# Kernel optimization log

Measured on AMD Instinct MI355X. Metric: run time of the kernel, lower is better.

Reference implementation:

```python
import jax, jax.numpy as jnp
import numpy as np

B, SEQ, H = 256, 200, 256
NFFT, HOP = 16, 8
FREQ = NFFT // 2 + 1          # 9
NSEG = SEQ // HOP + 1         # 26 (SEQ % HOP == 0 -> pad_len == 0)
FACTOR = 2


def _gelu(x):
    return jax.nn.gelu(x, approximate=False)  # torch nn.GELU / F.gelu default = exact erf


def _layernorm(x, w, b, eps=1e-12):
    u = x.mean(-1, keepdims=True)
    s = ((x - u) ** 2).mean(-1, keepdims=True)
    return w * (x - u) / jnp.sqrt(s + eps) + b


def _mixer(xr, xi, w1, b1, w2, b2):
    # complex MLP: einsum '...ijk,jkl->...ijl' with per-kept-dim weights
    e = lambda a, w: jnp.einsum('bijk,jkl->bijl', a, w)
    o1r = _gelu(e(xr, w1[0]) - e(xi, w1[1]) + b1[0])
    o1i = _gelu(e(xi, w1[0]) + e(xr, w1[1]) + b1[1])
    o2r = e(o1r, w2[0]) - e(o1i, w2[1]) + b2[0]
    # NOTE: faithful to the source bug: o1_image used in BOTH terms of o2_image
    o2i = e(o1i, w2[0]) + e(o1i, w2[1]) + b2[1]
    return o2r, o2i


def _stft(x):
    # torch.stft(n_fft=NFFT, hop=HOP, center=True, onesided=True, normalized=True,
    #            pad_mode='constant', window=None -> rectangular ones)
    pad = NFFT // 2
    xp = jnp.pad(x, ((0, 0), (pad, pad)))
    idx = jnp.arange(NSEG)[:, None] * HOP + jnp.arange(NFFT)[None, :]
    frames = xp[:, idx]                                    # [N, NSEG, NFFT]
    spec = jnp.fft.rfft(frames, axis=-1) * (NFFT ** -0.5)  # normalized=True
    return jnp.swapaxes(spec, -1, -2)                      # [N, FREQ, NSEG]


def _istft(spec):
    # torch.istft(center=True, normalized=True, rectangular window)
    n = spec.shape[0]
    frames = jnp.fft.irfft(jnp.swapaxes(spec, -1, -2) * (NFFT ** 0.5), n=NFFT, axis=-1)
    L = (NSEG - 1) * HOP + NFFT
    idx = (jnp.arange(NSEG)[:, None] * HOP + jnp.arange(NFFT)[None, :]).ravel()
    y = jnp.zeros((n, L), frames.dtype).at[:, idx].add(frames.reshape(n, -1))
    env = jnp.zeros((L,), frames.dtype).at[idx].add(1.0)   # window**2 overlap-add
    pad = NFFT // 2
    out_len = (NSEG - 1) * HOP                              # = SEQ
    return y[:, pad:pad + out_len] / env[pad:pad + out_len]


def setup_inputs() -> dict:
    key = jax.random.key(0)
    ks = jax.random.split(key, 24)
    p = lambda k, sh: jax.random.normal(k, sh, jnp.float32) * 0.02
    d = {}
    d["input_tensor"] = jax.random.normal(ks[0], (B, SEQ, H), jnp.float32)
    # grouped conv2d: weight [NSEG, 1, H, FREQ] -> stored as [NSEG, H, FREQ]
    d["conv_w"] = p(ks[1], (NSEG, H, FREQ)); d["conv_b"] = p(ks[2], (NSEG,))
    d["fm_w1"] = p(ks[3], (2, NSEG, FREQ, FREQ * FACTOR)); d["fm_b1"] = p(ks[4], (2, NSEG, FREQ * FACTOR))
    d["fm_w2"] = p(ks[5], (2, NSEG, FREQ * FACTOR, FREQ)); d["fm_b2"] = p(ks[6], (2, NSEG, FREQ))
    d["cm_w1"] = p(ks[7], (2, NSEG, H, H * FACTOR)); d["cm_b1"] = p(ks[8], (2, NSEG, H * FACTOR))
    d["cm_w2"] = p(ks[9], (2, NSEG, H * FACTOR, H)); d["cm_b2"] = p(ks[10], (2, NSEG, H))
    d["sm_w1"] = p(ks[11], (2, FREQ, NSEG, NSEG * FACTOR)); d["sm_b1"] = p(ks[12], (2, FREQ, NSEG * FACTOR))
    d["sm_w2"] = p(ks[13], (2, FREQ, NSEG * FACTOR, NSEG)); d["sm_b2"] = p(ks[14], (2, FREQ, NSEG))
    d["ln_w"] = jnp.ones((H,), jnp.float32); d["ln_b"] = jnp.zeros((H,), jnp.float32)
    d["ff_w1"] = p(ks[15], (H, 4 * H)); d["ff_b1"] = p(ks[16], (4 * H,))
    d["ff_w2"] = p(ks[17], (4 * H, H)); d["ff_b2"] = p(ks[18], (H,))
    d["ff_ln_w"] = jnp.ones((H,), jnp.float32); d["ff_ln_b"] = jnp.zeros((H,), jnp.float32)
    return d


def reference(input_tensor, conv_w, conv_b, fm_w1, fm_b1, fm_w2, fm_b2,
              cm_w1, cm_b1, cm_w2, cm_b2, sm_w1, sm_b1, sm_w2, sm_b2,
              ln_w, ln_b, ff_w1, ff_b1, ff_w2, ff_b2, ff_ln_w, ff_ln_b):
    b, seq, h = input_tensor.shape
    x = jnp.swapaxes(input_tensor, -1, -2).reshape(b * h, seq)  # pad_len == 0
    spec = _stft(x).reshape(b, h, FREQ, NSEG)
    xr, xi = spec.real, spec.imag
    xnorm = jnp.sqrt(xr ** 2 + xi ** 2)                         # [b,h,F,S]
    # grouped conv2d with full (H,FREQ) kernel == per-segment weighted sum
    w = jnp.einsum('bhfs,shf->bs', xnorm, conv_w) + conv_b
    w = w + jnp.exp(jnp.arange(1 - NSEG, 1, dtype=jnp.float32))  # exp decay bias
    xr = xr * w[:, None, None, :]
    xi = xi * w[:, None, None, :]
    # -> [b,h,S,F]: frequency mixing (kept=segment, mixed=freq)
    xr = jnp.swapaxes(xr, -1, -2); xi = jnp.swapaxes(xi, -1, -2)
    xr, xi = _mixer(xr, xi, fm_w1, fm_b1, fm_w2, fm_b2)
    # -> [b,F,S,h]: channel mixing (kept=segment, mixed=hidden)
    xr = jnp.swapaxes(xr, 1, 3); xi = jnp.swapaxes(xi, 1, 3)
    xr, xi = _mixer(xr, xi, cm_w1, cm_b1, cm_w2, cm_b2)
    # -> [b,h,F,S]: segment mixing (kept=freq, mixed=segment)
    xr = jnp.transpose(xr, (0, 3, 1, 2)); xi = jnp.transpose(xi, (0, 3, 1, 2))
    xr, xi = _mixer(xr, xi, sm_w1, sm_b1, sm_w2, sm_b2)
    spec = (xr + 1j * xi).reshape(b * h, FREQ, NSEG)
    y = _istft(spec)[:, :seq].reshape(b, h, seq)
    y = jnp.swapaxes(y, -1, -2)                                  # [b,seq,h]
    hs = _layernorm(y + input_tensor, ln_w, ln_b)                # dropout p=0
    ff = _gelu(hs @ ff_w1 + ff_b1) @ ff_w2 + ff_b2
    return _layernorm(ff + hs, ff_ln_w, ff_ln_b)
```

## Files before the change

kernel.cpp:

```cpp
#include <hip/hip_runtime.h>
#include <hip/hip_bf16.h>
#include <math.h>

typedef __hip_bfloat16 bf16;
typedef short bf16x8 __attribute__((ext_vector_type(8)));
typedef float f32x4 __attribute__((ext_vector_type(4)));

#define B_    256
#define SEQ_  200
#define H_    256
#define FREQ_ 9
#define NSEG_ 26
#define LDS64 64

__device__ __forceinline__ float ldb(const bf16* p, size_t i){ return __bfloat162float(p[i]); }
__device__ __forceinline__ void stb(bf16* p, size_t i, float v){ p[i] = __float2bfloat16(v); }
__device__ __forceinline__ short f2b(float v){ union{bf16 b; short s;} c; c.b = __float2bfloat16(v); return c.s; }
__device__ __forceinline__ float gelu_(float x){ return 0.5f*x*(1.0f+erff(x*0.7071067811865475f)); }

__device__ __constant__ float CT16[16] = {
  1.0f, 0.9238795325f, 0.7071067812f, 0.3826834324f, 0.0f, -0.3826834324f, -0.7071067812f, -0.9238795325f,
 -1.0f,-0.9238795325f,-0.7071067812f,-0.3826834324f, 0.0f,  0.3826834324f, 0.7071067812f,  0.9238795325f};
__device__ __constant__ float ST16[16] = {
  0.0f, 0.3826834324f, 0.7071067812f, 0.9238795325f, 1.0f,  0.9238795325f, 0.7071067812f,  0.3826834324f,
  0.0f,-0.3826834324f,-0.7071067812f,-0.9238795325f,-1.0f, -0.9238795325f,-0.7071067812f, -0.3826834324f};

__device__ __forceinline__ void gload16(const short* g, short* l){
  __builtin_amdgcn_global_load_lds(
      (const __attribute__((address_space(1))) unsigned int*)(const void*)g,
      (__attribute__((address_space(3))) unsigned int*)(void*)l, 16, 0, 0);
}

template<int ROWS>
__device__ __forceinline__ void stage_tile(short* lds, const short* src, int rstride, int tid){
  int rl = tid >> 3;
  int c  = tid & 7;
  #pragma unroll
  for(int p=0; p<ROWS/32; p++){
    int r = p*32 + rl;
    int csrc = c ^ (r & 7);
    gload16(src + (size_t)r*rstride + csrc*8, lds + r*LDS64 + c*8);
  }
}

__device__ __forceinline__ void mma_bk64(const short* lA, const short* lB, int wm, int wn,
                                         int lane, f32x4 acc[4][4]){
  int m_l = lane & 15, quad = lane >> 4;
  int sw = m_l & 7;
  #pragma unroll
  for(int ks=0; ks<64; ks+=32){
    int cs = (((ks>>3) + quad) ^ sw) * 8;
    bf16x8 a[4], b[4];
    #pragma unroll
    for(int i=0;i<4;i++) a[i] = *(const bf16x8*)&lA[(wm + i*16 + m_l)*LDS64 + cs];
    #pragma unroll
    for(int j=0;j<4;j++) b[j] = *(const bf16x8*)&lB[(wn + j*16 + m_l)*LDS64 + cs];
    #pragma unroll
    for(int i=0;i<4;i++)
      #pragma unroll
      for(int j=0;j<4;j++)
        acc[i][j] = __builtin_amdgcn_mfma_f32_16x16x32_bf16(a[i], b[j], acc[i][j], 0,0,0);
  }
}

__global__ __launch_bounds__(256) void k_prep_b1(const float* __restrict__ w1, short* __restrict__ B1t){
  int g = blockIdx.x;
  int jt = g & 7, ht = (g>>3)&3, p = (g>>5)&1, s = g>>6;
  __shared__ float tile[64][65];
  int t = threadIdx.x;
  const float* src = w1 + (size_t)p*3407872 + (size_t)s*131072;
  #pragma unroll
  for(int q=0;q<16;q++){
    int r = q*4 + (t>>6), c = t & 63;
    tile[r][c] = src[(size_t)(ht*64 + r)*512 + jt*64 + c];
  }
  __syncthreads();
  int n_l = t >> 2, kc = (t & 3)*16;
  short tA[16] __attribute__((aligned(16)));
  short tB[16] __attribute__((aligned(16)));
  #pragma unroll
  for(int i=0;i<16;i++){
    float v = tile[kc+i][n_l];
    tA[i] = (p==0) ? f2b(v) : f2b(-v);
    tB[i] = f2b(v);
  }
  int j = jt*64 + n_l, h = ht*64 + kc;
  size_t d1, d2;
  if(p==0){ d1 = ((size_t)(s*1024 + j))*512 + h;
            d2 = ((size_t)(s*1024 + 512 + j))*512 + 256 + h; }
  else    { d1 = ((size_t)(s*1024 + j))*512 + 256 + h;
            d2 = ((size_t)(s*1024 + 512 + j))*512 + h; }
  *(int4*)&B1t[d1] = *(int4*)&tA[0]; *(int4*)&B1t[d1+8] = *(int4*)&tA[8];
  *(int4*)&B1t[d2] = *(int4*)&tB[0]; *(int4*)&B1t[d2+8] = *(int4*)&tB[8];
}

__global__ __launch_bounds__(256) void k_prep_b2(const float* __restrict__ w2,
                                                 short* __restrict__ B2r, short* __restrict__ B2i){
  int g = blockIdx.x;
  int ht = g & 3, jt = (g>>2)&7, s = g>>5;
  __shared__ float t0[64][65], t1[64][65];
  int t = threadIdx.x;
  const float* s0 = w2 + (size_t)s*131072;
  const float* s1 = w2 + 3407872 + (size_t)s*131072;
  #pragma unroll
  for(int q=0;q<16;q++){
    int r = q*4 + (t>>6), c = t & 63;
    t0[r][c] = s0[(size_t)(jt*64 + r)*256 + ht*64 + c];
    t1[r][c] = s1[(size_t)(jt*64 + r)*256 + ht*64 + c];
  }
  __syncthreads();
  int n_l = t >> 2, jc = (t & 3)*16;
  short ta[16] __attribute__((aligned(16)));
  short tb[16] __attribute__((aligned(16)));
  short tc[16] __attribute__((aligned(16)));
  #pragma unroll
  for(int i=0;i<16;i++){
    float v0 = t0[jc+i][n_l], v1 = t1[jc+i][n_l];
    ta[i] = f2b(v0); tb[i] = f2b(-v1); tc[i] = f2b(v0+v1);
  }
  int n = ht*64 + n_l, j = jt*64 + jc;
  size_t dr = ((size_t)(s*256 + n))*1024 + j;
  size_t di = ((size_t)(s*256 + n))*512 + j;
  *(int4*)&B2r[dr]     = *(int4*)&ta[0]; *(int4*)&B2r[dr+8]     = *(int4*)&ta[8];
  *(int4*)&B2r[dr+512] = *(int4*)&tb[0]; *(int4*)&B2r[dr+520]   = *(int4*)&tb[8];
  *(int4*)&B2i[di]     = *(int4*)&tc[0]; *(int4*)&B2i[di+8]     = *(int4*)&tc[8];
}

__global__ __launch_bounds__(256) void k_transp(const float* __restrict__ src, short* __restrict__ dst,
                                                int R, int C){
  int ct = blockIdx.x % (C/64);
  int rt = blockIdx.x / (C/64);
  __shared__ float tile[64][65];
  int t = threadIdx.x;
  #pragma unroll
  for(int p=0;p<16;p++){
    int r = p*4 + (t>>6), c = t & 63;
    tile[r][c] = src[(size_t)(rt*64 + r)*C + ct*64 + c];
  }
  __syncthreads();
  int row_out = t >> 2, rc = (t & 3)*16;
  short tmp[16] __attribute__((aligned(16)));
  #pragma unroll
  for(int i=0;i<16;i++) tmp[i] = f2b(tile[rc+i][row_out]);
  size_t base = (size_t)(ct*64 + row_out)*R + rt*64 + rc;
  *(int4*)&dst[base] = *(int4*)&tmp[0]; *(int4*)&dst[base+8] = *(int4*)&tmp[8];
}

__global__ __launch_bounds__(256) void k_prep_sm(const float* __restrict__ w1, const float* __restrict__ w2,
                                                 short* __restrict__ B1sm, short* __restrict__ B2sm){
  int f = blockIdx.x;
  int t = threadIdx.x;
  for(int idx=t; idx<8192; idx+=256){
    int jp = idx >> 6, k = idx & 63;
    float v = 0.f;
    if(jp < 104){
      int j = (jp < 52) ? jp : jp - 52;
      if(k < 26){
        int s = k;
        v = (jp < 52) ? w1[f*1352 + s*52 + j] : w1[12168 + f*1352 + s*52 + j];
      } else if(k >= 32 && k < 58){
        int s = k - 32;
        v = (jp < 52) ? -w1[12168 + f*1352 + s*52 + j] : w1[f*1352 + s*52 + j];
      }
    }
    B1sm[(size_t)f*8192 + idx] = f2b(v);
  }
  for(int idx=t; idx<8192; idx+=256){
    int sop = idx >> 7, k = idx & 127;
    float v = 0.f;
    if(sop < 26){
      if(k < 52)       v = w2[f*1352 + k*26 + sop];
      else if(k < 104) v = -w2[12168 + f*1352 + (k-52)*26 + sop];
    } else if(sop < 52){
      int so = sop - 26;
      if(k >= 52 && k < 104)
        v = w2[f*1352 + (k-52)*26 + so] + w2[12168 + f*1352 + (k-52)*26 + so];
    }
    B2sm[(size_t)f*8192 + idx] = f2b(v);
  }
}

__global__ __launch_bounds__(256) void k_sfm(const float* __restrict__ inp,
                                             const float* __restrict__ cw, const float* __restrict__ cb,
                                             const float* __restrict__ w1, const float* __restrict__ bb1,
                                             const float* __restrict__ w2, const float* __restrict__ bb2,
                                             bf16* __restrict__ oR, bf16* __restrict__ oI){
  int blk = blockIdx.x; int b = blk / NSEG_; int s = blk % NSEG_; int h = threadIdx.x;
  __shared__ float2 lw1[162], lw2[162], lb1[18], lb2[9];
  __shared__ float red[256];
  for(int i=h; i<162; i+=256){
    lw1[i] = make_float2(w1[s*162+i], w1[4212 + s*162+i]);
    lw2[i] = make_float2(w2[s*162+i], w2[4212 + s*162+i]);
  }
  if(h < 18) lb1[h] = make_float2(bb1[s*18+h], bb1[468 + s*18+h]);
  if(h < 9)  lb2[h] = make_float2(bb2[s*9+h],  bb2[234 + s*9+h]);

  float xv[16];
  int t0 = s*8 - 8;
  #pragma unroll
  for(int k=0;k<16;k++){
    int t = t0 + k;
    xv[k] = (t>=0 && t<SEQ_) ? inp[(size_t)(b*SEQ_+t)*H_ + h] : 0.0f;
  }
  float xr[9], xi[9];
  float acc = 0.f;
  #pragma unroll
  for(int f=0;f<FREQ_;f++){
    float ar=0.f, ai=0.f;
    #pragma unroll
    for(int k=0;k<16;k++){
      int m = (f*k) & 15;
      ar += xv[k]*CT16[m];
      ai -= xv[k]*ST16[m];
    }
    xr[f] = 0.25f*ar; xi[f] = 0.25f*ai;
    acc += sqrtf(xr[f]*xr[f] + xi[f]*xi[f]) * cw[(s*H_+h)*FREQ_ + f];
  }

  red[h] = acc; __syncthreads();
  for(int off=128; off>0; off>>=1){ if(h<off) red[h] += red[h+off]; __syncthreads(); }
  float wv = red[0] + cb[s] + __expf((float)(s - (NSEG_-1)));
  #pragma unroll
  for(int f=0;f<9;f++){ xr[f] *= wv; xi[f] *= wv; }

  float gr[18], gi[18];
  #pragma unroll
  for(int j=0;j<18;j++){
    float hr = lb1[j].x, hi = lb1[j].y;
    #pragma unroll
    for(int f=0;f<9;f++){
      float2 ww = lw1[f*18+j];
      hr += xr[f]*ww.x - xi[f]*ww.y;
      hi += xi[f]*ww.x + xr[f]*ww.y;
    }
    gr[j] = gelu_(hr); gi[j] = gelu_(hi);
  }
  #pragma unroll
  for(int f=0;f<9;f++){
    float orr = lb2[f].x, oii = lb2[f].y;
    #pragma unroll
    for(int j=0;j<18;j++){
      float2 ww = lw2[j*9+f];
      orr += gr[j]*ww.x - gi[j]*ww.y;
      oii += gi[j]*ww.x + gi[j]*ww.y;
    }
    size_t o = ((size_t)(s*B_+b)*FREQ_+f)*H_ + h;
    stb(oR, o, orr); stb(oI, o, oii);
  }
}

__global__ __launch_bounds__(256) void k_cm1(const bf16* __restrict__ Xr, const bf16* __restrict__ Xi,
                                             const short* __restrict__ B1t, const float* __restrict__ b1bias,
                                             short* __restrict__ H, int half){
  int nt = blockIdx.x & 7, mt = (blockIdx.x >> 3) % 9, s = blockIdx.x / 72;
  int tid = threadIdx.x, lane = tid & 63, wave = tid >> 6;
  int wm = (wave & 1)*64, wn = (wave >> 1)*64;
  __shared__ __align__(16) short lA[128*LDS64];
  __shared__ __align__(16) short lB[128*LDS64];
  f32x4 acc[4][4];
  #pragma unroll
  for(int i=0;i<4;i++)
    #pragma unroll
    for(int j=0;j<4;j++) acc[i][j] = (f32x4){0.f,0.f,0.f,0.f};
  int rowbase = half*1152 + mt*128;
  const short* Bbase = B1t + ((size_t)(s*1024 + nt*128))*512;
  for(int k0=0; k0<512; k0+=64){
    const short* Asrc = (k0 < 256)
      ? (const short*)(Xr + ((size_t)(s*2304 + rowbase))*256 + k0)
      : (const short*)(Xi + ((size_t)(s*2304 + rowbase))*256 + (k0-256));
    stage_tile<128>(lA, Asrc, 256, tid);
    stage_tile<128>(lB, Bbase + k0, 512, tid);
    __syncthreads();
    mma_bk64(lA, lB, wm, wn, lane, acc);
    __syncthreads();
  }
  int m_l = lane & 15, quad = lane >> 4;
  #pragma unroll
  for(int i=0;i<4;i++){
    #pragma unroll
    for(int j=0;j<4;j++){
      int n = nt*128 + wn + j*16 + m_l;
      float bias = (n < 512) ? b1bias[s*512 + n] : b1bias[13312 + s*512 + (n-512)];
      #pragma unroll
      for(int r=0;r<4;r++){
        int mrow = wm + i*16 + quad*4 + r;
        float v = gelu_(acc[i][j][r] + bias);
        H[((size_t)(s*1152 + mt*128 + mrow))*1024 + n] = f2b(v);
      }
    }
  }
}

__global__ __launch_bounds__(256) void k_cm2(const short* __restrict__ H,
                                             const short* __restrict__ B2r, const short* __restrict__ B2i,
                                             const float* __restrict__ b2bias,
                                             bf16* __restrict__ oR, bf16* __restrict__ oI, int half){
  int nt = blockIdx.x & 3, mt = (blockIdx.x>>2) % 9, s = blockIdx.x / 36;
  int tid = threadIdx.x, lane = tid & 63, wave = tid >> 6;
  int wm = (wave & 1)*64, wn = (wave >> 1)*64;
  bool isOi = nt >= 2;
  int n0 = (nt & 1)*128;
  int K = isOi ? 512 : 1024;
  int Aoff = isOi ? 512 : 0;
  int Bstride = isOi ? 512 : 1024;
  const short* Bb = isOi ? (B2i + ((size_t)(s*256 + n0))*512) : (B2r + ((size_t)(s*256 + n0))*1024);
  const short* Ab = H + ((size_t)(s*1152 + mt*128))*1024 + Aoff;
  __shared__ __align__(16) short lA[128*LDS64];
  __shared__ __align__(16) short lB[128*LDS64];
  f32x4 acc[4][4];
  #pragma unroll
  for(int i=0;i<4;i++)
    #pragma unroll
    for(int j=0;j<4;j++) acc[i][j] = (f32x4){0.f,0.f,0.f,0.f};
  for(int k0=0; k0<K; k0+=64){
    stage_tile<128>(lA, Ab + k0, 1024, tid);
    stage_tile<128>(lB, Bb + k0, Bstride, tid);
    __syncthreads();
    mma_bk64(lA, lB, wm, wn, lane, acc);
    __syncthreads();
  }
  int m_l = lane & 15, quad = lane >> 4;
  bf16* outp = isOi ? oI : oR;
  #pragma unroll
  for(int i=0;i<4;i++){
    #pragma unroll
    for(int j=0;j<4;j++){
      int n = n0 + wn + j*16 + m_l;
      float bias = b2bias[(isOi ? 6656 : 0) + s*256 + n];
      #pragma unroll
      for(int r=0;r<4;r++){
        int mrow = wm + i*16 + quad*4 + r;
        int rowg = half*1152 + mt*128 + mrow;
        stb(outp, ((size_t)rowg*NSEG_ + s)*256 + n, acc[i][j][r] + bias);
      }
    }
  }
}

#define LDX 72
#define LDG 136
__global__ __launch_bounds__(256) void k_smm(const bf16* __restrict__ iR, const bf16* __restrict__ iI,
                                             const short* __restrict__ B1sm, const short* __restrict__ B2sm,
                                             const float* __restrict__ bb1, const float* __restrict__ bb2,
                                             bf16* __restrict__ oR, bf16* __restrict__ oI){
  int blk = blockIdx.x;
  int f  = blk % 9;
  int hh = (blk/9) & 1;
  int bq = blk / 18;
  int t = threadIdx.x, lane = t & 63, wave = t >> 6;
  int m_l = lane & 15, quad = lane >> 4;
  __shared__ __align__(16) short sm[18432 + 8704];
  __shared__ float lb1[128];
  short* lX  = sm;
  short* lB1 = sm + 128*LDX;
  short* lG  = sm;
  short* lB2 = sm + 18432;
  int rbase = (bq*9 + f)*26;

  #pragma unroll
  for(int it=0; it<4; it++){
    int idx = it*256 + t;
    int r = idx >> 3, c = idx & 7;
    *(int4*)&lB1[r*LDX + c*8] = *(const int4*)&B1sm[(size_t)f*8192 + r*64 + c*8];
  }
  #pragma unroll
  for(int it=0; it<4; it++){
    int idx = it*256 + t;
    int r = idx >> 4, c = idx & 15;
    *(int4*)&lB2[r*LDG + c*8] = *(const int4*)&B2sm[(size_t)f*8192 + r*128 + c*8];
  }
  if(t < 128) lb1[t] = (t < 52) ? bb1[f*52 + t] : (t < 104 ? bb1[468 + f*52 + (t-52)] : 0.f);

  int hl = t & 127, g = t >> 7;
  #pragma unroll
  for(int it=0; it<13; it++){
    int a   = it*2 + g;
    int arr = a >= 13;
    int pr  = arr ? a-13 : a;
    int s0  = pr*2;
    const bf16* src = arr ? iI : iR;
    unsigned v0 = *(const unsigned short*)&src[((size_t)(rbase+s0  ))*256 + hh*128 + hl];
    unsigned v1 = *(const unsigned short*)&src[((size_t)(rbase+s0+1))*256 + hh*128 + hl];
    *(unsigned*)&lX[hl*LDX + arr*32 + s0] = v0 | (v1 << 16);
  }
  {
    int zb = g ? 58 : 26;
    #pragma unroll
    for(int i=0;i<3;i++) *(unsigned*)&lX[hl*LDX + zb + i*2] = 0u;
  }
  __syncthreads();

  int h0 = wave*32;
  f32x4 acc1[2][8];
  #pragma unroll
  for(int i=0;i<2;i++)
    #pragma unroll
    for(int j=0;j<8;j++) acc1[i][j] = (f32x4){0.f,0.f,0.f,0.f};
  #pragma unroll
  for(int ks=0; ks<64; ks+=32){
    bf16x8 av[2], bv[8];
    #pragma unroll
    for(int i=0;i<2;i++) av[i] = *(const bf16x8*)&lX[(h0 + i*16 + m_l)*LDX + ks + quad*8];
    #pragma unroll
    for(int j=0;j<8;j++) bv[j] = *(const bf16x8*)&lB1[(j*16 + m_l)*LDX + ks + quad*8];
    #pragma unroll
    for(int i=0;i<2;i++)
      #pragma unroll
      for(int j=0;j<8;j++)
        acc1[i][j] = __builtin_amdgcn_mfma_f32_16x16x32_bf16(av[i], bv[j], acc1[i][j], 0,0,0);
  }
  __syncthreads();

  #pragma unroll
  for(int i=0;i<2;i++){
    #pragma unroll
    for(int j=0;j<8;j++){
      int jp = j*16 + m_l;
      float bias = lb1[jp];
      #pragma unroll
      for(int r=0;r<4;r++){
        int hrow = h0 + i*16 + quad*4 + r;
        lG[hrow*LDG + jp] = f2b(gelu_(acc1[i][j][r] + bias));
      }
    }
  }
  __syncthreads();

  f32x4 acc2[2][4];
  #pragma unroll
  for(int i=0;i<2;i++)
    #pragma unroll
    for(int j=0;j<4;j++) acc2[i][j] = (f32x4){0.f,0.f,0.f,0.f};
  #pragma unroll
  for(int ks=0; ks<128; ks+=32){
    bf16x8 av[2], bv[4];
    #pragma unroll
    for(int i=0;i<2;i++) av[i] = *(const bf16x8*)&lG[(h0 + i*16 + m_l)*LDG + ks + quad*8];
    #pragma unroll
    for(int j=0;j<4;j++) bv[j] = *(const bf16x8*)&lB2[(j*16 + m_l)*LDG + ks + quad*8];
    #pragma unroll
    for(int i=0;i<2;i++)
      #pragma unroll
      for(int j=0;j<4;j++)
        acc2[i][j] = __builtin_amdgcn_mfma_f32_16x16x32_bf16(av[i], bv[j], acc2[i][j], 0,0,0);
  }

  #pragma unroll
  for(int j=0;j<4;j++){
    int sop = j*16 + m_l;
    if(sop < 52){
      int arr = sop >= 26;
      int so  = sop - (arr ? 26 : 0);
      float bias = bb2[(arr ? 234 : 0) + f*26 + so];
      bf16* outp = arr ? oI : oR;
      #pragma unroll
      for(int i=0;i<2;i++){
        int h = hh*128 + h0 + i*16 + quad*4;
        short pk[4] __attribute__((aligned(8)));
        #pragma unroll
        for(int r=0;r<4;r++) pk[r] = f2b(acc2[i][j][r] + bias);
        *(int2*)&outp[((size_t)(rbase + so))*256 + h] = *(const int2*)&pk[0];
      }
    }
  }
}

__global__ __launch_bounds__(256) void k_ist(const bf16* __restrict__ iR, const bf16* __restrict__ iI,
                                             const float* __restrict__ inp,
                                             const float* __restrict__ lnw, const float* __restrict__ lnb,
                                             float* __restrict__ hs, bf16* __restrict__ hsb){
  int blk = blockIdx.x; int b = blk / SEQ_; int t = blk % SEQ_; int h = threadIdx.x;
  int l = t + 8;
  int s2 = l >> 3, k2 = l & 7;
  int s1 = s2 - 1, k1 = k2 + 8;
  float acc = 0.f;
  #pragma unroll
  for(int p=0;p<2;p++){
    int s = p ? s2 : s1;
    int k = p ? k2 : k1;
    size_t base = (size_t)(b*FREQ_)*NSEG_;
    float v = ldb(iR, (base + 0*NSEG_ + s)*256 + h);
    float a8 = ldb(iR, (base + 8*NSEG_ + s)*256 + h);
    v += (k & 1) ? -a8 : a8;
    #pragma unroll
    for(int f=1;f<8;f++){
      int m = (f*k) & 15;
      float rr = ldb(iR, (base + f*NSEG_ + s)*256 + h);
      float ii = ldb(iI, (base + f*NSEG_ + s)*256 + h);
      v += 2.f*(rr*CT16[m] - ii*ST16[m]);
    }
    acc += 0.25f*v;
  }
  float z = 0.5f*acc + inp[(size_t)(b*SEQ_+t)*H_ + h];

  __shared__ float red[256];
  red[h] = z; __syncthreads();
  for(int off=128; off>0; off>>=1){ if(h<off) red[h] += red[h+off]; __syncthreads(); }
  float u = red[0] * (1.f/256.f);
  __syncthreads();
  float d = z - u;
  red[h] = d*d; __syncthreads();
  for(int off=128; off>0; off>>=1){ if(h<off) red[h] += red[h+off]; __syncthreads(); }
  float var = red[0] * (1.f/256.f);
  float o = lnw[h]*d*rsqrtf(var + 1e-12f) + lnb[h];
  size_t oi = (size_t)(b*SEQ_+t)*H_ + h;
  hs[oi] = o;
  stb(hsb, oi, o);
}

__global__ __launch_bounds__(256) void k_ff1m(const short* __restrict__ hsb, const short* __restrict__ fw1t,
                                              const float* __restrict__ fb1, short* __restrict__ hid, int row0){
  int nt = blockIdx.x & 7, mt = blockIdx.x >> 3;
  int tid = threadIdx.x, lane = tid & 63, wave = tid >> 6;
  int wm = (wave & 1)*64, wn = (wave >> 1)*64;
  __shared__ __align__(16) short lA[128*LDS64];
  __shared__ __align__(16) short lB[128*LDS64];
  f32x4 acc[4][4];
  #pragma unroll
  for(int i=0;i<4;i++)
    #pragma unroll
    for(int j=0;j<4;j++) acc[i][j] = (f32x4){0.f,0.f,0.f,0.f};
  const short* Ab = hsb + ((size_t)(row0 + mt*128))*256;
  const short* Bb = fw1t + ((size_t)(nt*128))*256;
  for(int k0=0; k0<256; k0+=64){
    stage_tile<128>(lA, Ab + k0, 256, tid);
    stage_tile<128>(lB, Bb + k0, 256, tid);
    __syncthreads();
    mma_bk64(lA, lB, wm, wn, lane, acc);
    __syncthreads();
  }
  int m_l = lane & 15, quad = lane >> 4;
  #pragma unroll
  for(int i=0;i<4;i++){
    #pragma unroll
    for(int j=0;j<4;j++){
      int n = nt*128 + wn + j*16 + m_l;
      float bias = fb1[n];
      #pragma unroll
      for(int r=0;r<4;r++){
        int mrow = wm + i*16 + quad*4 + r;
        hid[((size_t)(mt*128 + mrow))*1024 + n] = f2b(gelu_(acc[i][j][r] + bias));
      }
    }
  }
}

__global__ __launch_bounds__(256) void k_ff2m(const short* __restrict__ hid, const short* __restrict__ fw2t,
                                              const float* __restrict__ fb2, const float* __restrict__ hs,
                                              const float* __restrict__ lnw, const float* __restrict__ lnb,
                                              float* __restrict__ out, int row0){
  int mt = blockIdx.x;
  int tid = threadIdx.x, lane = tid & 63, wave = tid >> 6;
  int wn = wave*64;
  __shared__ __align__(16) short lA[64*LDS64];
  __shared__ __align__(16) short lB[256*LDS64];
  __shared__ float ssum[64][4], ssq[64][4];
  f32x4 acc[4][4];
  #pragma unroll
  for(int i=0;i<4;i++)
    #pragma unroll
    for(int j=0;j<4;j++) acc[i][j] = (f32x4){0.f,0.f,0.f,0.f};
  const short* Ab = hid + ((size_t)(mt*64))*1024;
  for(int k0=0; k0<1024; k0+=64){
    stage_tile<64>(lA, Ab + k0, 1024, tid);
    stage_tile<256>(lB, fw2t + k0, 1024, tid);
    __syncthreads();
    mma_bk64(lA, lB, 0, wn, lane, acc);
    __syncthreads();
  }
  int m_l = lane & 15, quad = lane >> 4;
  int rowg0 = row0 + mt*64;
  #pragma unroll
  for(int i=0;i<4;i++){
    #pragma unroll
    for(int j=0;j<4;j++){
      int col = wn + j*16 + m_l;
      float bias = fb2[col];
      #pragma unroll
      for(int r=0;r<4;r++){
        int mrow = i*16 + quad*4 + r;
        acc[i][j][r] += bias + hs[(size_t)(rowg0+mrow)*256 + col];
      }
    }
  }
  #pragma unroll
  for(int i=0;i<4;i++){
    #pragma unroll
    for(int r=0;r<4;r++){
      float sv = 0.f, sq = 0.f;
      #pragma unroll
      for(int j=0;j<4;j++){ float v = acc[i][j][r]; sv += v; sq += v*v; }
      #pragma unroll
      for(int msk=1; msk<16; msk<<=1){ sv += __shfl_xor(sv, msk); sq += __shfl_xor(sq, msk); }
      if(m_l == 0){ int mrow = i*16 + quad*4 + r; ssum[mrow][wave] = sv; ssq[mrow][wave] = sq; }
    }
  }
  __syncthreads();
  if(tid < 64){
    float s1 = ssum[tid][0]+ssum[tid][1]+ssum[tid][2]+ssum[tid][3];
    float s2 = ssq[tid][0]+ssq[tid][1]+ssq[tid][2]+ssq[tid][3];
    float mean = s1*(1.f/256.f);
    float var  = s2*(1.f/256.f) - mean*mean;
    ssum[tid][0] = mean;
    ssq[tid][0]  = rsqrtf(var + 1e-12f);
  }
  __syncthreads();
  #pragma unroll
  for(int i=0;i<4;i++){
    #pragma unroll
    for(int j=0;j<4;j++){
      int col = wn + j*16 + m_l;
      float gw = lnw[col], gb = lnb[col];
      #pragma unroll
      for(int r=0;r<4;r++){
        int mrow = i*16 + quad*4 + r;
        float mean = ssum[mrow][0], inv = ssq[mrow][0];
        out[(size_t)(rowg0+mrow)*256 + col] = (acc[i][j][r] - mean)*inv*gw + gb;
      }
    }
  }
}

extern "C" void kernel_launch(void* const* d_in, const int* in_sizes, int n_in,
                              void* d_out, int out_size, void* d_ws, size_t ws_size,
                              hipStream_t stream){
  const float* inp    = (const float*)d_in[0];
  const float* conv_w = (const float*)d_in[1];
  const float* conv_b = (const float*)d_in[2];
  const float* fm_w1  = (const float*)d_in[3];
  const float* fm_b1  = (const float*)d_in[4];
  const float* fm_w2  = (const float*)d_in[5];
  const float* fm_b2  = (const float*)d_in[6];
  const float* cm_w1  = (const float*)d_in[7];
  const float* cm_b1  = (const float*)d_in[8];
  const float* cm_w2  = (const float*)d_in[9];
  const float* cm_b2  = (const float*)d_in[10];
  const float* sm_w1  = (const float*)d_in[11];
  const float* sm_b1  = (const float*)d_in[12];
  const float* sm_w2  = (const float*)d_in[13];
  const float* sm_b2  = (const float*)d_in[14];
  const float* ln_w   = (const float*)d_in[15];
  const float* ln_b   = (const float*)d_in[16];
  const float* ff_w1  = (const float*)d_in[17];
  const float* ff_b1  = (const float*)d_in[18];
  const float* ff_w2  = (const float*)d_in[19];
  const float* ff_b2  = (const float*)d_in[20];
  const float* ffln_w = (const float*)d_in[21];
  const float* ffln_b = (const float*)d_in[22];
  float* out = (float*)d_out;

  const size_t NS = (size_t)B_ * NSEG_ * FREQ_ * H_;
  const size_t HN = (size_t)NSEG_ * 1152 * 1024;
  short* ws = (short*)d_ws;
  bf16*  b0   = (bf16*)ws;
  bf16*  b1   = (bf16*)(ws + NS);
  bf16*  b2   = (bf16*)(ws + 2*NS);
  bf16*  b3   = (bf16*)(ws + 3*NS);
  short* H    = ws + 4*NS;
  short* B1t  = H + HN;
  short* B2r  = B1t + (size_t)26*1024*512;
  short* B2i  = B2r + (size_t)26*256*1024;
  short* fw1t = B2i + (size_t)26*256*512;
  short* fw2t = fw1t + 262144;
  short* B1sm = fw2t + 262144;
  short* B2sm = B1sm + 73728;
  float* hs   = (float*)b0;
  bf16*  hsb  = (bf16*)H;
  short* hid  = (short*)b2;

  k_prep_b1<<<1664, 256, 0, stream>>>(cm_w1, B1t);
  k_prep_b2<<<832,  256, 0, stream>>>(cm_w2, B2r, B2i);
  k_transp <<<64,   256, 0, stream>>>(ff_w1, fw1t, 256, 1024);
  k_transp <<<64,   256, 0, stream>>>(ff_w2, fw2t, 1024, 256);
  k_prep_sm<<<9,    256, 0, stream>>>(sm_w1, sm_w2, B1sm, B2sm);

  k_sfm<<<B_*NSEG_, 256, 0, stream>>>(inp, conv_w, conv_b, fm_w1, fm_b1, fm_w2, fm_b2, b2, b3);
  for(int half=0; half<2; half++){
    k_cm1<<<26*72, 256, 0, stream>>>(b2, b3, B1t, cm_b1, H, half);
    k_cm2<<<26*36, 256, 0, stream>>>(H, B2r, B2i, cm_b2, b0, b1, half);
  }
  k_smm<<<B_*2*FREQ_, 256, 0, stream>>>(b0, b1, B1sm, B2sm, sm_b1, sm_b2, b2, b3);
  k_ist<<<B_*SEQ_,  256, 0, stream>>>(b2, b3, inp, ln_w, ln_b, hs, hsb);
  for(int c=0; c<2; c++){
    int row0 = c*25600;
    k_ff1m<<<1600, 256, 0, stream>>>((const short*)hsb, fw1t, ff_b1, hid, row0);
    k_ff2m<<<400,  256, 0, stream>>>(hid, fw2t, ff_b2, hs, ffln_w, ffln_b, out, row0);
  }
}
```

Measured before the change: 953.1 us.

## Move frequency-mixer complex MLP onto bf16 MFMA with prepacked real-block weights

Replaces the scalar per-thread complex MLP in the STFT/frequency-mix kernel with two small bf16 MFMA GEMMs. Activations are staged through LDS, and the complex weights come from a new prep kernel that packs them into real block matrices, including the source bug's o2i term. The aim is to cut the large FP32 FMA count per thread. In exchange it adds LDS traffic, extra barriers, bf16 rounding of the intermediates, and zero-padded K/N dimensions (18→32, 36→64).

```diff
diff --git a/kernel.cpp b/kernel.cpp
--- a/kernel.cpp
+++ b/kernel.cpp
@@ -16,6 +16,7 @@
 __device__ __forceinline__ float ldb(const bf16* p, size_t i){ return __bfloat162float(p[i]); }
 __device__ __forceinline__ void stb(bf16* p, size_t i, float v){ p[i] = __float2bfloat16(v); }
 __device__ __forceinline__ short f2b(float v){ union{bf16 b; short s;} c; c.b = __float2bfloat16(v); return c.s; }
+__device__ __forceinline__ unsigned short f2bu(float v){ union{bf16 b; unsigned short s;} c; c.b = __float2bfloat16(v); return c.s; }
 __device__ __forceinline__ float gelu_(float x){ return 0.5f*x*(1.0f+erff(x*0.7071067811865475f)); }
 
 __device__ __constant__ float CT16[16] = {
@@ -180,27 +181,75 @@
   }
 }
 
-__global__ __launch_bounds__(256) void k_sfm(const float* __restrict__ inp,
-                                             const float* __restrict__ cw, const float* __restrict__ cb,
-                                             const float* __restrict__ w1, const float* __restrict__ bb1,
-                                             const float* __restrict__ w2, const float* __restrict__ bb2,
-                                             bf16* __restrict__ oR, bf16* __restrict__ oI){
-  int blk = blockIdx.x; int b = blk / NSEG_; int s = blk % NSEG_; int h = threadIdx.x;
-  __shared__ float2 lw1[162], lw2[162], lb1[18], lb2[9];
+__global__ __launch_bounds__(256) void k_prep_fm(const float* __restrict__ w1, const float* __restrict__ w2,
+                                                 short* __restrict__ B1fm, short* __restrict__ B2fm){
+  int s = blockIdx.x;
+  int t = threadIdx.x;
+  for(int idx=t; idx<1536; idx+=256){
+    int n = idx >> 5, k = idx & 31;
+    float v = 0.f;
+    if(n < 18){
+      if(k < 9)       v = w1[s*162 + k*18 + n];
+      else if(k < 18) v = -w1[4212 + s*162 + (k-9)*18 + n];
+    } else if(n < 36){
+      int j = n - 18;
+      if(k < 9)       v = w1[4212 + s*162 + k*18 + j];
+      else if(k < 18) v = w1[s*162 + (k-9)*18 + j];
+    }
+    B1fm[s*1536 + idx] = f2b(v);
+  }
+  for(int idx=t; idx<2048; idx+=256){
+    int n = idx >> 6, k = idx & 63;
+    float v = 0.f;
+    if(n < 9){
+      if(k < 18)      v = w2[s*162 + k*9 + n];
+      else if(k < 36) v = -w2[4212 + s*162 + (k-18)*9 + n];
+    } else if(n < 18){
+      int f = n - 9;
+      if(k >= 18 && k < 36)
+        v = w2[s*162 + (k-18)*9 + f] + w2[4212 + s*162 + (k-18)*9 + f];
+    }
+    B2fm[s*2048 + idx] = f2b(v);
+  }
+}
+
+#define LX1 40
+#define LG1 72
+__global__ __launch_bounds__(256) void k_sfm2(const float* __restrict__ inp,
+                                              const float* __restrict__ cw, const float* __restrict__ cb,
+                                              const short* __restrict__ B1fm, const short* __restrict__ B2fm,
+                                              const float* __restrict__ bb1, const float* __restrict__ bb2,
+                                              bf16* __restrict__ oR, bf16* __restrict__ oI){
+  int blk = blockIdx.x; int b = blk / NSEG_; int s = blk % NSEG_; int t = threadIdx.x;
+  int lane = t & 63, wave = t >> 6, m_l = lane & 15, quad = lane >> 4;
+  __shared__ __align__(16) short sm[20736];
   __shared__ float red[256];
-  for(int i=h; i<162; i+=256){
-    lw1[i] = make_float2(w1[s*162+i], w1[4212 + s*162+i]);
-    lw2[i] = make_float2(w2[s*162+i], w2[4212 + s*162+i]);
-  }
-  if(h < 18) lb1[h] = make_float2(bb1[s*18+h], bb1[468 + s*18+h]);
-  if(h < 9)  lb2[h] = make_float2(bb2[s*9+h],  bb2[234 + s*9+h]);
+  __shared__ float lb1f[48];
+  short* lX  = sm;
+  short* lB1 = sm + 10240;
+  short* lG  = sm;
+  short* lB2 = sm + 18432;
+
+  {
+    const short* src1 = B1fm + s*1536;
+    for(int idx=t; idx<768; idx+=256){
+      int r = idx >> 4, c = idx & 15;
+      *(unsigned*)&lB1[r*LX1 + c*2] = *(const unsigned*)&src1[r*32 + c*2];
+    }
+    const short* src2 = B2fm + s*2048;
+    for(int idx=t; idx<1024; idx+=256){
+      int r = idx >> 5, c = idx & 31;
+      *(unsigned*)&lB2[r*LG1 + c*2] = *(const unsigned*)&src2[r*64 + c*2];
+    }
+    if(t < 48) lb1f[t] = (t < 18) ? bb1[s*18 + t] : (t < 36 ? bb1[468 + s*18 + (t-18)] : 0.f);
+  }
 
   float xv[16];
   int t0 = s*8 - 8;
   #pragma unroll
   for(int k=0;k<16;k++){
-    int t = t0 + k;
-    xv[k] = (t>=0 && t<SEQ_) ? inp[(size_t)(b*SEQ_+t)*H_ + h] : 0.0f;
+    int tt = t0 + k;
+    xv[k] = (tt>=0 && tt<SEQ_) ? inp[(size_t)(b*SEQ_+tt)*H_ + t] : 0.0f;
   }
   float xr[9], xi[9];
   float acc = 0.f;
@@ -214,38 +263,101 @@
       ai -= xv[k]*ST16[m];
     }
     xr[f] = 0.25f*ar; xi[f] = 0.25f*ai;
-    acc += sqrtf(xr[f]*xr[f] + xi[f]*xi[f]) * cw[(s*H_+h)*FREQ_ + f];
-  }
-
-  red[h] = acc; __syncthreads();
-  for(int off=128; off>0; off>>=1){ if(h<off) red[h] += red[h+off]; __syncthreads(); }
+    acc += sqrtf(xr[f]*xr[f] + xi[f]*xi[f]) * cw[(s*H_+t)*FREQ_ + f];
+  }
+
+  red[t] = acc; __syncthreads();
+  for(int off=128; off>0; off>>=1){ if(t<off) red[t] += red[t+off]; __syncthreads(); }
   float wv = red[0] + cb[s] + __expf((float)(s - (NSEG_-1)));
-  #pragma unroll
-  for(int f=0;f<9;f++){ xr[f] *= wv; xi[f] *= wv; }
-
-  float gr[18], gi[18];
-  #pragma unroll
-  for(int j=0;j<18;j++){
-    float hr = lb1[j].x, hi = lb1[j].y;
-    #pragma unroll
-    for(int f=0;f<9;f++){
-      float2 ww = lw1[f*18+j];
-      hr += xr[f]*ww.x - xi[f]*ww.y;
-      hi += xi[f]*ww.x + xr[f]*ww.y;
-    }
-    gr[j] = gelu_(hr); gi[j] = gelu_(hi);
-  }
-  #pragma unroll
-  for(int f=0;f<9;f++){
-    float orr = lb2[f].x, oii = lb2[f].y;
-    #pragma unroll
-    for(int j=0;j<18;j++){
-      float2 ww = lw2[j*9+f];
-      orr += gr[j]*ww.x - gi[j]*ww.y;
-      oii += gi[j]*ww.x + gi[j]*ww.y;
-    }
-    size_t o = ((size_t)(s*B_+b)*FREQ_+f)*H_ + h;
-    stb(oR, o, orr); stb(oI, o, oii);
+
+  {
+    float vb[32];
+    #pragma unroll
+    for(int f=0;f<9;f++){ vb[f] = xr[f]*wv; vb[9+f] = xi[f]*wv; }
+    #pragma unroll
+    for(int k=18;k<32;k++) vb[k] = 0.f;
+    #pragma unroll
+    for(int c=0;c<16;c++){
+      unsigned u = (unsigned)f2bu(vb[2*c]) | ((unsigned)f2bu(vb[2*c+1]) << 16);
+      *(unsigned*)&lX[t*LX1 + c*2] = u;
+    }
+  }
+  __syncthreads();
+
+  int h0 = wave*64;
+  f32x4 acc1[4][3];
+  #pragma unroll
+  for(int i=0;i<4;i++)
+    #pragma unroll
+    for(int j=0;j<3;j++) acc1[i][j] = (f32x4){0.f,0.f,0.f,0.f};
+  {
+    bf16x8 a1[4], b1v[3];
+    #pragma unroll
+    for(int i=0;i<4;i++) a1[i] = *(const bf16x8*)&lX[(h0 + i*16 + m_l)*LX1 + quad*8];
+    #pragma unroll
+    for(int j=0;j<3;j++) b1v[j] = *(const bf16x8*)&lB1[(j*16 + m_l)*LX1 + quad*8];
+    #pragma unroll
+    for(int i=0;i<4;i++)
+      #pragma unroll
+      for(int j=0;j<3;j++)
+        acc1[i][j] = __builtin_amdgcn_mfma_f32_16x16x32_bf16(a1[i], b1v[j], acc1[i][j], 0,0,0);
+  }
+  __syncthreads();
+
+  #pragma unroll
+  for(int i=0;i<4;i++){
+    #pragma unroll
+    for(int j=0;j<3;j++){
+      int n = j*16 + m_l;
+      float bias = lb1f[n];
+      #pragma unroll
+      for(int r=0;r<4;r++){
+        int row = h0 + i*16 + quad*4 + r;
+        lG[row*LG1 + n] = f2b(gelu_(acc1[i][j][r] + bias));
+      }
+    }
+  }
+  #pragma unroll
+  for(int c=0;c<8;c++) *(unsigned*)&lG[t*LG1 + 48 + c*2] = 0u;
+  __syncthreads();
+
+  f32x4 acc2[4][2];
+  #pragma unroll
+  for(int i=0;i<4;i++)
+    #pragma unroll
+    for(int j=0;j<2;j++) acc2[i][j] = (f32x4){0.f,0.f,0.f,0.f};
+  #pragma unroll
+  for(int ks=0; ks<64; ks+=32){
+    bf16x8 a2[4], b2v[2];
+    #pragma unroll
+    for(int i=0;i<4;i++) a2[i] = *(const bf16x8*)&lG[(h0 + i*16 + m_l)*LG1 + ks + quad*8];
+    #pragma unroll
+    for(int j=0;j<2;j++) b2v[j] = *(const bf16x8*)&lB2[(j*16 + m_l)*LG1 + ks + quad*8];
+    #pragma unroll
+    for(int i=0;i<4;i++)
+      #pragma unroll
+      for(int j=0;j<2;j++)
+        acc2[i][j] = __builtin_amdgcn_mfma_f32_16x16x32_bf16(a2[i], b2v[j], acc2[i][j], 0,0,0);
+  }
+
+  #pragma unroll
+  for(int j=0;j<2;j++){
+    int n = j*16 + m_l;
+    if(n < 18){
+      bool isI = n >= 9;
+      int f = isI ? n-9 : n;
+      float bias = isI ? bb2[234 + s*9 + f] : bb2[s*9 + f];
+      bf16* outp = isI ? oI : oR;
+      size_t base = ((size_t)(s*B_ + b)*FREQ_ + f)*H_;
+      #pragma unroll
+      for(int i=0;i<4;i++){
+        int h = h0 + i*16 + quad*4;
+        short pk[4] __attribute__((aligned(8)));
+        #pragma unroll
+        for(int r=0;r<4;r++) pk[r] = f2b(acc2[i][j][r] + bias);
+        *(int2*)&outp[base + h] = *(const int2*)&pk[0];
+      }
+    }
   }
 }
 
@@ -664,6 +776,8 @@
   short* fw2t = fw1t + 262144;
   short* B1sm = fw2t + 262144;
   short* B2sm = B1sm + 73728;
+  short* B1fm = B2sm + 73728;
+  short* B2fm = B1fm + 39936;
   float* hs   = (float*)b0;
   bf16*  hsb  = (bf16*)H;
   short* hid  = (short*)b2;
@@ -673,8 +787,9 @@
   k_transp <<<64,   256, 0, stream>>>(ff_w1, fw1t, 256, 1024);
   k_transp <<<64,   256, 0, stream>>>(ff_w2, fw2t, 1024, 256);
   k_prep_sm<<<9,    256, 0, stream>>>(sm_w1, sm_w2, B1sm, B2sm);
-
-  k_sfm<<<B_*NSEG_, 256, 0, stream>>>(inp, conv_w, conv_b, fm_w1, fm_b1, fm_w2, fm_b2, b2, b3);
+  k_prep_fm<<<26,   256, 0, stream>>>(fm_w1, fm_w2, B1fm, B2fm);
+
+  k_sfm2<<<B_*NSEG_, 256, 0, stream>>>(inp, conv_w, conv_b, B1fm, B2fm, fm_b1, fm_b2, b2, b3);
   for(int half=0; half<2; half++){
     k_cm1<<<26*72, 256, 0, stream>>>(b2, b3, B1t, cm_b1, H, half);
     k_cm2<<<26*36, 256, 0, stream>>>(H, B2r, B2i, cm_b2, b0, b1, half);
```

Result: faster. 915.5 us (-3.9%).
